# Performance work log

Hardware: AMD Instinct MI355X
Metric: run time of the kernel (lower is better)

Reference implementation:

```python
import jax, jax.numpy as jnp
import numpy as np

B, S, K, N = 4, 2048, 4096, 4096


def setup_inputs() -> dict:
    key = jax.random.key(0)
    kx, kw = jax.random.split(key)
    # int8 activations and weights in [-127, 127), matching torch.randint(-127,127,...)
    x = jax.random.randint(kx, (B, S, K), -127, 127, dtype=jnp.int32).astype(jnp.int8)
    weight = jax.random.randint(kw, (N, K), -127, 127, dtype=jnp.int32).astype(jnp.int8)
    bias = jnp.zeros((1, N), dtype=jnp.int32)
    out_scale = jnp.ones((), dtype=jnp.float32)
    bias_scale = jnp.ones((), dtype=jnp.float32)
    return {"x": x, "weight": weight, "bias": bias,
            "out_scale": out_scale, "bias_scale": bias_scale}


def reference(x, weight, bias, out_scale, bias_scale):
    # Flatten leading dims: [B, S, K] -> [M, K]
    x_shape = x.shape
    x2 = x.reshape(-1, x_shape[-1])
    acc = jax.lax.dot_general(
        x2, weight,
        dimension_numbers=(((1,), (1,)), ((), ())),
        preferred_element_type=jnp.int32,
    )  # [M, N] int32
    # Fused epilogue: y = round(out_scale * acc + bias_scale * bias) -> int32
    y = jnp.round(acc.astype(jnp.float32) * out_scale
                  + bias.astype(jnp.float32) * bias_scale).astype(jnp.int32)
    return y.reshape(*x_shape[:-1], -1)
```

## Files before the change

kernel.cpp:

```cpp
#include <hip/hip_runtime.h>
#include <stdint.h>


typedef int v4i __attribute__((ext_vector_type(4)));

#define BM 256
#define BN 256
#define BK 128
#define KK 4096
#define KT (KK / BK)

__global__ __launch_bounds__(256)
void pack_i32_to_i8(const v4i* __restrict__ src, int* __restrict__ dst, int n4) {
    int i = blockIdx.x * blockDim.x + threadIdx.x;
    if (i >= n4) return;
    v4i a = src[i];
    dst[i] = (a[0] & 0xff) | ((a[1] & 0xff) << 8) | ((a[2] & 0xff) << 16) | (a[3] << 24);
}

__device__ __forceinline__ void gld_lds16(const void* g, void* lds) {
    __builtin_amdgcn_global_load_lds(
        (const __attribute__((address_space(1))) unsigned int*)g,
        (__attribute__((address_space(3))) unsigned int*)lds,
        16, 0, 0);
}

#define MFMA_I8 __builtin_amdgcn_mfma_i32_16x16x64_i8

#define COMPUTE_SLICE(XO) do {                                                    \
    v4i a[8], b[4];                                                               \
    b[0] = *(const v4i*)(sBb + rowB + 0 * 2048 + (XO));                           \
    a[0] = *(const v4i*)(sAb + rowA + 0 * 2048 + (XO));                           \
    b[1] = *(const v4i*)(sBb + rowB + 1 * 2048 + (XO));                           \
    b[2] = *(const v4i*)(sBb + rowB + 2 * 2048 + (XO));                           \
    b[3] = *(const v4i*)(sBb + rowB + 3 * 2048 + (XO));                           \
    _Pragma("unroll")                                                             \
    for (int i = 1; i < 8; ++i)                                                   \
        a[i] = *(const v4i*)(sAb + rowA + i * 2048 + (XO));                       \
    _Pragma("unroll")                                                             \
    for (int i = 0; i < 8; ++i)                                                   \
        _Pragma("unroll")                                                         \
        for (int j = 0; j < 4; ++j)                                               \
            acc[i][j] = MFMA_I8(a[i], b[j], acc[i][j], 0, 0, 0);                  \
} while (0)

__global__ __launch_bounds__(512, 2)
void w8a8_gemm_kernel(const int8_t* __restrict__ X,
                      const int8_t* __restrict__ W,
                      const int*    __restrict__ bias,
                      const float*  __restrict__ out_scale_p,
                      const float*  __restrict__ bias_scale_p,
                      int*          __restrict__ Y,
                      int M, int N)
{
    __shared__ __align__(16) int8_t sA[2 * BM * BK];
    __shared__ __align__(16) int8_t sB[2 * BN * BK];

    const int tid = threadIdx.x;

    const int nbx = N / BN;
    const int nby = M / BM;
    int bx, by;
    {
        const int wg = blockIdx.x;
        if (nbx == 16 && nby == 32) {
            const int x = wg & 7;
            const int k = wg >> 3;
            bx = ((x & 1) << 3) | (k & 7);
            by = ((x >> 1) << 3) | (k >> 3);
        } else { bx = wg % nbx; by = wg / nbx; }
    }
    const int bn = bx * BN;
    const int bm = by * BM;

    const float out_scale  = *out_scale_p;
    const float bias_scale = *bias_scale_p;

    const int8_t* Abase = X + (size_t)bm * KK;
    const int8_t* Bbase = W + (size_t)bn * KK;

    const int r0  = tid >> 3;
    const int j0  = tid & 7;
    const int sw  = (j0 ^ (r0 & 7)) << 4;
    const size_t gOff = (size_t)r0 * KK + sw;
    const int  lOff = tid << 4;

#define STAGE(gbase, lds, t, h) do {                                              \
        const int8_t* _g = (gbase) + (size_t)((h) * 128) * KK                     \
                                   + (size_t)(t) * BK + gOff;                     \
        int8_t* _l = (lds) + (((t) & 1) << 15) + ((h) << 14) + lOff;              \
        gld_lds16(_g,                  _l);                                       \
        gld_lds16(_g + (size_t)64 * KK, _l + 8192);                               \
    } while (0)

    const int w    = tid >> 6;
    const int l    = tid & 63;
    const int wmw  = w >> 2;
    const int wnw  = w & 3;
    const int tm   = l & 15;
    const int quad = l >> 4;
    const int s3   = tm & 7;
    const int xo0  = ( quad      ^ s3) << 4;
    const int xo1  = ((quad + 4) ^ s3) << 4;
    const int rowA = ((wmw << 7) + tm) << 7;
    const int rowB = ((wnw << 6) + tm) << 7;

    v4i acc[8][4];
    const v4i vz = {0, 0, 0, 0};
#pragma unroll
    for (int i = 0; i < 8; ++i)
#pragma unroll
        for (int j = 0; j < 4; ++j)
            acc[i][j] = vz;

    STAGE(Abase, sA, 0, 0); STAGE(Abase, sA, 0, 1);
    STAGE(Bbase, sB, 0, 0); STAGE(Bbase, sB, 0, 1);
    __syncthreads();

#pragma unroll 2
    for (int t = 0; t < KT; ++t) {
        const int bo = (t & 1) << 15;
        const int8_t* sAb = sA + bo;
        const int8_t* sBb = sB + bo;

        if (t + 1 < KT) {
            STAGE(Abase, sA, t + 1, 0); STAGE(Abase, sA, t + 1, 1);
            STAGE(Bbase, sB, t + 1, 0); STAGE(Bbase, sB, t + 1, 1);
        }
        __builtin_amdgcn_sched_barrier(0);

        COMPUTE_SLICE(xo0);
        COMPUTE_SLICE(xo1);

        __syncthreads();
    }
#undef STAGE

    float bb[4];
#pragma unroll
    for (int j = 0; j < 4; ++j)
        bb[j] = (float)bias[bn + (wnw << 6) + (j << 4) + tm] * bias_scale;
#pragma unroll
    for (int i = 0; i < 8; ++i) {
        const int mb = bm + (wmw << 7) + (i << 4) + (quad << 2);
#pragma unroll
        for (int r = 0; r < 4; ++r) {
            int* yrow = Y + (size_t)(mb + r) * N + bn + (wnw << 6) + tm;
#pragma unroll
            for (int j = 0; j < 4; ++j) {
                const float v = (float)acc[i][j][r] * out_scale + bb[j];
                yrow[j << 4] = (int)rintf(v);
            }
        }
    }
}

extern "C" void kernel_launch(void* const* d_in, const int* in_sizes, int n_in,
                              void* d_out, int out_size, void* d_ws, size_t ws_size,
                              hipStream_t stream) {
    const int* x32 = (const int*)d_in[0];
    const int* w32 = (const int*)d_in[1];
    const int*    bias = (const int*)d_in[2];
    const float*  os   = (const float*)d_in[3];
    const float*  bs   = (const float*)d_in[4];
    int* out = (int*)d_out;

    const int K = KK;
    const int M = in_sizes[0] / K;
    const int N = in_sizes[1] / K;
    const int nx = in_sizes[0];
    const int nw = in_sizes[1];

    int8_t* x8 = (int8_t*)d_ws;
    int8_t* w8 = x8 + (size_t)nx;

    pack_i32_to_i8<<<dim3(nx / 4 / 256), dim3(256), 0, stream>>>((const v4i*)x32, (int*)x8, nx / 4);
    pack_i32_to_i8<<<dim3(nw / 4 / 256), dim3(256), 0, stream>>>((const v4i*)w32, (int*)w8, nw / 4);

    dim3 grid((N / BN) * (M / BM));
    dim3 block(512);
    hipLaunchKernelGGL(w8a8_gemm_kernel, grid, block, 0, stream,
                       x8, w8, bias, os, bs, out, M, N);
}
```

Baseline: 393.6 us.

## Switch to 32x32x32 i8 MFMA with staggered LDS-read/MFMA schedule per wave group

Replaces the 16x16x64 int8 MFMA tiling with 32x32x32 int8 MFMAs, so each wave computes a 4x2 grid of 32x32 tiles with 16-element accumulators. Fewer LDS fragment reads are needed per MFMA, which lowers LDS traffic for each unit of compute. The two wave groups get differently staggered read/compute orders so their LDS reads and MFMAs interleave. The epilogue is rewritten to match the 32x32 output layout. The cost is a different register footprint and a row-scattered store pattern.

New measurement: 402.3 us. 1.02x slower.

```diff
diff --git a/kernel.cpp b/kernel.cpp
--- a/kernel.cpp
+++ b/kernel.cpp
@@ -2,7 +2,8 @@
 #include <stdint.h>
 
 
-typedef int v4i __attribute__((ext_vector_type(4)));
+typedef int v4i  __attribute__((ext_vector_type(4)));
+typedef int v16i __attribute__((ext_vector_type(16)));
 
 #define BM 256
 #define BN 256
@@ -25,23 +26,28 @@
         16, 0, 0);
 }
 
-#define MFMA_I8 __builtin_amdgcn_mfma_i32_16x16x64_i8
-
-#define COMPUTE_SLICE(XO) do {                                                    \
-    v4i a[8], b[4];                                                               \
-    b[0] = *(const v4i*)(sBb + rowB + 0 * 2048 + (XO));                           \
-    a[0] = *(const v4i*)(sAb + rowA + 0 * 2048 + (XO));                           \
-    b[1] = *(const v4i*)(sBb + rowB + 1 * 2048 + (XO));                           \
-    b[2] = *(const v4i*)(sBb + rowB + 2 * 2048 + (XO));                           \
-    b[3] = *(const v4i*)(sBb + rowB + 3 * 2048 + (XO));                           \
-    _Pragma("unroll")                                                             \
-    for (int i = 1; i < 8; ++i)                                                   \
-        a[i] = *(const v4i*)(sAb + rowA + i * 2048 + (XO));                       \
-    _Pragma("unroll")                                                             \
-    for (int i = 0; i < 8; ++i)                                                   \
-        _Pragma("unroll")                                                         \
-        for (int j = 0; j < 4; ++j)                                               \
-            acc[i][j] = MFMA_I8(a[i], b[j], acc[i][j], 0, 0, 0);                  \
+#define MFMA32 __builtin_amdgcn_mfma_i32_32x32x32_i8
+
+#define RD(S, ks) do {                                                            \
+    const int sa_ = ((((ks) << 1) | hi) ^ s3a) << 4;                              \
+    const int sb_ = ((((ks) << 1) | hi) ^ s3b) << 4;                              \
+    fr[S][0] = *(const v4i*)(sAb + rowAb +     0 + sa_);                          \
+    fr[S][1] = *(const v4i*)(sAb + rowAb +  4096 + sa_);                          \
+    fr[S][2] = *(const v4i*)(sAb + rowAb +  8192 + sa_);                          \
+    fr[S][3] = *(const v4i*)(sAb + rowAb + 12288 + sa_);                          \
+    fr[S][4] = *(const v4i*)(sBb + rowBb +     0 + sb_);                          \
+    fr[S][5] = *(const v4i*)(sBb + rowBb +  4096 + sb_);                          \
+} while (0)
+
+#define MM(S) do {                                                                \
+    acc[0][0] = MFMA32(fr[S][0], fr[S][4], acc[0][0], 0, 0, 0);                   \
+    acc[0][1] = MFMA32(fr[S][0], fr[S][5], acc[0][1], 0, 0, 0);                   \
+    acc[1][0] = MFMA32(fr[S][1], fr[S][4], acc[1][0], 0, 0, 0);                   \
+    acc[1][1] = MFMA32(fr[S][1], fr[S][5], acc[1][1], 0, 0, 0);                   \
+    acc[2][0] = MFMA32(fr[S][2], fr[S][4], acc[2][0], 0, 0, 0);                   \
+    acc[2][1] = MFMA32(fr[S][2], fr[S][5], acc[2][1], 0, 0, 0);                   \
+    acc[3][0] = MFMA32(fr[S][3], fr[S][4], acc[3][0], 0, 0, 0);                   \
+    acc[3][1] = MFMA32(fr[S][3], fr[S][5], acc[3][1], 0, 0, 0);                   \
 } while (0)
 
 __global__ __launch_bounds__(512, 2)
@@ -95,23 +101,25 @@
 
     const int w    = tid >> 6;
     const int l    = tid & 63;
+    const int pg   = w >> 2;
     const int wmw  = w >> 2;
     const int wnw  = w & 3;
-    const int tm   = l & 15;
-    const int quad = l >> 4;
-    const int s3   = tm & 7;
-    const int xo0  = ( quad      ^ s3) << 4;
-    const int xo1  = ((quad + 4) ^ s3) << 4;
-    const int rowA = ((wmw << 7) + tm) << 7;
-    const int rowB = ((wnw << 6) + tm) << 7;
-
-    v4i acc[8][4];
-    const v4i vz = {0, 0, 0, 0};
-#pragma unroll
-    for (int i = 0; i < 8; ++i)
-#pragma unroll
-        for (int j = 0; j < 4; ++j)
-            acc[i][j] = vz;
+    const int ln31 = l & 31;
+    const int hi   = l >> 5;
+    const int arow = (wmw << 7) + ln31;
+    const int brow = (wnw << 6) + ln31;
+    const int s3a  = arow & 7;
+    const int s3b  = brow & 7;
+    const int rowAb = arow << 7;
+    const int rowBb = brow << 7;
+
+    v16i acc[4][2];
+    const v16i vz16 = {0,0,0,0, 0,0,0,0, 0,0,0,0, 0,0,0,0};
+#pragma unroll
+    for (int i = 0; i < 4; ++i)
+#pragma unroll
+        for (int j = 0; j < 2; ++j)
+            acc[i][j] = vz16;
 
     STAGE(Abase, sA, 0, 0); STAGE(Abase, sA, 0, 1);
     STAGE(Bbase, sB, 0, 0); STAGE(Bbase, sB, 0, 1);
@@ -129,27 +137,40 @@
         }
         __builtin_amdgcn_sched_barrier(0);
 
-        COMPUTE_SLICE(xo0);
-        COMPUTE_SLICE(xo1);
+        {
+            v4i fr[2][6];
+            if (pg == 0) {
+                RD(0, 0); MM(0);
+                RD(1, 1); MM(1);
+                RD(0, 2); MM(0);
+                RD(1, 3); MM(1);
+            } else {
+                RD(0, 0);
+                RD(1, 1); MM(0);
+                RD(0, 2); MM(1);
+                RD(1, 3); MM(0);
+                MM(1);
+            }
+        }
 
         __syncthreads();
     }
 #undef STAGE
 
-    float bb[4];
-#pragma unroll
-    for (int j = 0; j < 4; ++j)
-        bb[j] = (float)bias[bn + (wnw << 6) + (j << 4) + tm] * bias_scale;
-#pragma unroll
-    for (int i = 0; i < 8; ++i) {
-        const int mb = bm + (wmw << 7) + (i << 4) + (quad << 2);
-#pragma unroll
-        for (int r = 0; r < 4; ++r) {
-            int* yrow = Y + (size_t)(mb + r) * N + bn + (wnw << 6) + tm;
-#pragma unroll
-            for (int j = 0; j < 4; ++j) {
-                const float v = (float)acc[i][j][r] * out_scale + bb[j];
-                yrow[j << 4] = (int)rintf(v);
+    float bbv[2];
+#pragma unroll
+    for (int j = 0; j < 2; ++j)
+        bbv[j] = (float)bias[bn + (wnw << 6) + (j << 5) + ln31] * bias_scale;
+#pragma unroll
+    for (int mt = 0; mt < 4; ++mt) {
+#pragma unroll
+        for (int r = 0; r < 16; ++r) {
+            const int m = bm + (wmw << 7) + (mt << 5) + (hi << 2) + (r & 3) + ((r >> 2) << 3);
+            int* yrow = Y + (size_t)m * N + bn + (wnw << 6) + ln31;
+#pragma unroll
+            for (int nt = 0; nt < 2; ++nt) {
+                const float v = (float)acc[mt][nt][r] * out_scale + bbv[nt];
+                yrow[nt << 5] = (int)rintf(v);
             }
         }
     }
```
